# Kernel tuning notes

Measured on AMD Instinct MI355X. Metric: run time of the kernel, lower is better.

Reference implementation:

```python
import jax, jax.numpy as jnp
import numpy as np

B, S, I, H, C = 256, 128, 512, 1024, 10
VOCAB = S  # nn.Embedding(seq_length, input_dim)


def _lstm_dir(embeds_tbi, W, b):
    """Run an LSTM over time. embeds_tbi: [S,B,I]; W: [4H, I+H] stacked (g,i,f,o); b: [4H]."""
    h0 = jnp.zeros((B, H), jnp.float32)
    c0 = jnp.zeros((B, H), jnp.float32)

    def step(carry, x_t):
        c, h = carry
        xh = jnp.concatenate([x_t, h], axis=1)          # [B, I+H]
        z = xh @ W.T + b                                 # [B, 4H]
        g, i, f, o = jnp.split(z, 4, axis=1)
        g = jnp.tanh(g)
        i = jax.nn.sigmoid(i)
        f = jax.nn.sigmoid(f)
        o = jax.nn.sigmoid(o)
        new_c = g * i + c * f
        new_h = jnp.tanh(new_c) * o
        return (new_c, new_h), None

    (c_T, h_T), _ = jax.lax.scan(step, (c0, h0), embeds_tbi)
    return h_T


def setup_inputs() -> dict:
    key = jax.random.key(0)
    ks = jax.random.split(key, 8)
    x = jax.random.randint(ks[0], (B, S), 0, VOCAB)
    embed = jax.random.normal(ks[1], (VOCAB, I), jnp.float32) * 0.5
    scale = 1.0 / np.sqrt(I + H)
    fwd_W = jax.random.normal(ks[2], (4 * H, I + H), jnp.float32) * scale  # stacked g,i,f,o
    fwd_b = jax.random.normal(ks[3], (4 * H,), jnp.float32) * 0.02
    bwd_W = jax.random.normal(ks[4], (4 * H, I + H), jnp.float32) * scale
    bwd_b = jax.random.normal(ks[5], (4 * H,), jnp.float32) * 0.02
    p_w = jax.random.normal(ks[6], (C, 2 * H), jnp.float32) * (1.0 / np.sqrt(2 * H))
    p_b = jax.random.normal(ks[7], (C,), jnp.float32) * 0.02
    return {"x": x, "embed": embed, "fwd_W": fwd_W, "fwd_b": fwd_b,
            "bwd_W": bwd_W, "bwd_b": bwd_b, "p_w": p_w, "p_b": p_b}


def reference(x, embed, fwd_W, fwd_b, bwd_W, bwd_b, p_w, p_b):
    embeds = embed[x]                       # [B,S,I]
    emb_t = jnp.transpose(embeds, (1, 0, 2))  # [S,B,I]
    h_fwd = _lstm_dir(emb_t, fwd_W, fwd_b)
    h_bwd = _lstm_dir(emb_t[::-1], bwd_W, bwd_b)
    h_comb = jnp.concatenate([h_fwd, h_bwd], axis=1)  # [B,2H]
    return jax.nn.log_softmax(h_comb @ p_w.T + p_b, axis=1)
```

## Files before the change

### kernel.cpp

```cpp
#include <hip/hip_runtime.h>
#include <hip/hip_bf16.h>
#include <math.h>

#define B 256
#define S 128
#define I_DIM 512
#define H 1024
#define C 10
#define WROW 1536

#define LDS_H 131072

typedef float f32x4 __attribute__((ext_vector_type(4), may_alias));
typedef __bf16 bf16x8 __attribute__((ext_vector_type(8), may_alias));
typedef unsigned int u32x4 __attribute__((ext_vector_type(4), may_alias));
typedef unsigned long long u64;
typedef unsigned long long __attribute__((may_alias)) u64a;

__device__ __forceinline__ unsigned short f2bf(float f) {
    union { float f; unsigned u; } a; a.f = f;
    return (unsigned short)((a.u + 0x7fffu + ((a.u >> 16) & 1u)) >> 16);
}
__device__ __forceinline__ float sigf(float v) { return 1.0f / (1.0f + __expf(-v)); }
__device__ __forceinline__ float tanh_fast(float v) { return 1.0f - 2.0f / (1.0f + __expf(2.0f * v)); }

__global__ void wf_build(const float* __restrict__ fwd_W,
                         const float* __restrict__ bwd_W,
                         __hip_bfloat16* __restrict__ wF) {
    int gid = blockIdx.x * 256 + threadIdx.x;
    int lane = gid & 63, kk = (gid >> 6) & 31, nsub = (gid >> 11) & 255, d = gid >> 19;
    int n_gl = nsub * 16 + (lane & 15);
    int j = n_gl >> 2, g = n_gl & 3;
    int k = kk * 32 + (lane >> 4) * 8;
    const float* W = d ? bwd_W : fwd_W;
    const float* src = W + (size_t)(g * 1024 + j) * WROW + I_DIM + k;
    ushort4 lo = make_ushort4(f2bf(src[0]), f2bf(src[1]), f2bf(src[2]), f2bf(src[3]));
    ushort4 hi = make_ushort4(f2bf(src[4]), f2bf(src[5]), f2bf(src[6]), f2bf(src[7]));
    ushort4* dst = (ushort4*)(wF + (size_t)gid * 8);
    dst[0] = lo; dst[1] = hi;
}

__global__ void projp_kernel(const float* __restrict__ embed,
                             const float* __restrict__ fwd_W,
                             const float* __restrict__ fwd_b,
                             const float* __restrict__ bwd_W,
                             const float* __restrict__ bwd_b,
                             float* __restrict__ projP) {
    __shared__ float wrows[16][516];
    int d  = blockIdx.x >> 8;
    int nc = blockIdx.x & 255;
    int n0 = nc * 16;
    const float* W    = d ? bwd_W : fwd_W;
    const float* bias = d ? bwd_b : fwd_b;
    int tid = threadIdx.x;
    for (int idx = tid; idx < 16 * 512; idx += 256) {
        int r = idx >> 9, k = idx & 511;
        wrows[r][k] = W[(n0 + r) * WROW + k];
    }
    __syncthreads();
    for (int o = tid; o < 128 * 16; o += 256) {
        int v = o >> 4, r = o & 15;
        const float* er = embed + v * I_DIM;
        float s = bias[n0 + r];
        for (int k = 0; k < I_DIM; k++) s += er[k] * wrows[r][k];
        int n = n0 + r;
        int g = n >> 10, j = n & 1023;
        projP[(((size_t)d * 1024 + j) * 128 + v) * 4 + g] = s;
    }
}

__global__ __launch_bounds__(512, 1) void step_kernel(
        const int* __restrict__ x,
        const __hip_bfloat16* __restrict__ wF,
        const float* __restrict__ projP,
        __hip_bfloat16* __restrict__ hbuf,
        float* __restrict__ cws,
        int t) {
    extern __shared__ char smem[];
    const int bid = blockIdx.x;
    const int d = bid >> 7, bt = (bid >> 5) & 3, jt = bid & 31;
    const int tid = threadIdx.x, wid = tid >> 6, lane = tid & 63;
    const int l15 = lane & 15, l4 = lane >> 4;
    const int b0 = bt * 64;
    const size_t dBH = (size_t)d * B * H;

    if (t > 0) {
        const __hip_bfloat16* hr = hbuf + (size_t)(t & 1) * 2 * B * H + dBH + (size_t)b0 * H;
#pragma unroll
        for (int i = 0; i < 16; i++) {
            int flat = i * 512 + tid;
            int row = flat >> 7, c16 = flat & 127;
            u32x4 v = *(const u32x4*)(hr + (size_t)row * H + c16 * 8);
            *(u32x4*)(smem + row * 2048 + ((c16 * 16) ^ ((row & 7) << 4))) = v;
        }
        __syncthreads();
    }

    f32x4 acc[4] = {};
    if (t > 0) {
        const __hip_bfloat16* wp = wF + (size_t)(d * 256 + jt * 8 + wid) * 16384;
        int brow[4], bswz[4];
#pragma unroll
        for (int bs = 0; bs < 4; bs++) {
            int row = bs * 16 + l15;
            brow[bs] = row * 2048;
            bswz[bs] = (row & 7) << 4;
        }
        bf16x8 Acur = *(const bf16x8*)(wp + lane * 8);
        bf16x8 Bcur[4];
#pragma unroll
        for (int bs = 0; bs < 4; bs++)
            Bcur[bs] = *(const bf16x8*)(smem + brow[bs] + ((l4 * 16) ^ bswz[bs]));
#pragma unroll
        for (int kk = 0; kk < 32; kk++) {
            bf16x8 A = Acur;
            bf16x8 B0 = Bcur[0], B1 = Bcur[1], B2 = Bcur[2], B3 = Bcur[3];
            if (kk < 31) {
                Acur = *(const bf16x8*)(wp + (kk + 1) * 512 + lane * 8);
                int koff = (kk + 1) * 64 + l4 * 16;
#pragma unroll
                for (int bs = 0; bs < 4; bs++)
                    Bcur[bs] = *(const bf16x8*)(smem + brow[bs] + (koff ^ bswz[bs]));
            }
            acc[0] = __builtin_amdgcn_mfma_f32_16x16x32_bf16(A, B0, acc[0], 0, 0, 0);
            acc[1] = __builtin_amdgcn_mfma_f32_16x16x32_bf16(A, B1, acc[1], 0, 0, 0);
            acc[2] = __builtin_amdgcn_mfma_f32_16x16x32_bf16(A, B2, acc[2], 0, 0, 0);
            acc[3] = __builtin_amdgcn_mfma_f32_16x16x32_bf16(A, B3, acc[3], 0, 0, 0);
        }
    }

    const int tt = d ? (S - 1 - t) : t;
    const int j = jt * 32 + wid * 4 + l4;
    const f32x4* pp = (const f32x4*)projP + ((size_t)d * 1024 + j) * 128;
    f32x4 pj[4];
#pragma unroll
    for (int bs = 0; bs < 4; bs++) {
        int v = x[(b0 + bs * 16 + l15) * S + tt];
        pj[bs] = pp[v];
    }

    float* cp = cws + ((size_t)bid * 512 + tid) * 4;
    f32x4 cv = {0.f, 0.f, 0.f, 0.f};
    if (t > 0) cv = *(const f32x4*)cp;

    float hnv[4];
#pragma unroll
    for (int bs = 0; bs < 4; bs++) {
        float zg = acc[bs][0] + pj[bs][0];
        float zi = acc[bs][1] + pj[bs][1];
        float zf = acc[bs][2] + pj[bs][2];
        float zo = acc[bs][3] + pj[bs][3];
        float gg = tanh_fast(zg);
        float ii = sigf(zi);
        float ff = sigf(zf);
        float oo = sigf(zo);
        float cn = gg * ii + cv[bs] * ff;
        cv[bs] = cn;
        hnv[bs] = tanh_fast(cn) * oo;
    }
    *(f32x4*)cp = cv;

    unsigned plo = (unsigned)f2bf(hnv[0]) | ((unsigned)f2bf(hnv[1]) << 16);
    unsigned phi = (unsigned)f2bf(hnv[2]) | ((unsigned)f2bf(hnv[3]) << 16);
    unsigned short o4[4];
#pragma unroll
    for (int p = 0; p < 4; p++) {
        int src = p * 16 + l15;
        unsigned vlo = __shfl(plo, src);
        unsigned vhi = __shfl(phi, src);
        unsigned sel = (l4 < 2) ? vlo : vhi;
        o4[p] = (l4 & 1) ? (unsigned short)(sel >> 16) : (unsigned short)(sel & 0xffffu);
    }
    u64 hv = (u64)o4[0] | ((u64)o4[1] << 16) | ((u64)o4[2] << 32) | ((u64)o4[3] << 48);
    __hip_bfloat16* hw = hbuf + (size_t)((t + 1) & 1) * 2 * B * H + dBH
                         + (size_t)(b0 + lane) * H + jt * 32 + wid * 4;
    *(u64a*)hw = hv;
}

__global__ void head_kernel(const __hip_bfloat16* __restrict__ hbuf,
                            const float* __restrict__ p_w,
                            const float* __restrict__ p_b,
                            float* __restrict__ out) {
    int b = blockIdx.x;
    int lane = threadIdx.x;
    float part[C];
#pragma unroll
    for (int cc = 0; cc < C; cc++) part[cc] = 0.0f;
    for (int jj = lane; jj < 2 * H; jj += 64) {
        float hv = (jj < H)
            ? __bfloat162float(hbuf[(size_t)b * H + jj])
            : __bfloat162float(hbuf[(size_t)B * H + (size_t)b * H + jj - H]);
#pragma unroll
        for (int cc = 0; cc < C; cc++) part[cc] += hv * p_w[cc * 2 * H + jj];
    }
#pragma unroll
    for (int cc = 0; cc < C; cc++) {
        float v = part[cc];
        for (int off = 32; off; off >>= 1) v += __shfl_down(v, off);
        part[cc] = v;
    }
    if (lane == 0) {
        float lg[C];
        float m = -1e30f;
        for (int cc = 0; cc < C; cc++) {
            lg[cc] = part[cc] + p_b[cc];
            m = fmaxf(m, lg[cc]);
        }
        float s = 0.0f;
        for (int cc = 0; cc < C; cc++) s += expf(lg[cc] - m);
        float lse = logf(s) + m;
        for (int cc = 0; cc < C; cc++) out[b * C + cc] = lg[cc] - lse;
    }
}

extern "C" void kernel_launch(void* const* d_in, const int* in_sizes, int n_in,
                              void* d_out, int out_size, void* d_ws, size_t ws_size,
                              hipStream_t stream) {
    const int*   x     = (const int*)d_in[0];
    const float* embed = (const float*)d_in[1];
    const float* fwd_W = (const float*)d_in[2];
    const float* fwd_b = (const float*)d_in[3];
    const float* bwd_W = (const float*)d_in[4];
    const float* bwd_b = (const float*)d_in[5];
    const float* p_w   = (const float*)d_in[6];
    const float* p_b   = (const float*)d_in[7];
    float* outp = (float*)d_out;

    char* ws = (char*)d_ws;
    __hip_bfloat16* wF = (__hip_bfloat16*)ws;  ws += (size_t)2 * 256 * 16384 * 2;
    float* projP = (float*)ws;                 ws += (size_t)2 * 1024 * 128 * 4 * 4;
    __hip_bfloat16* hbuf = (__hip_bfloat16*)ws; ws += (size_t)2 * 2 * B * H * 2;
    float* cws = (float*)ws;                   ws += (size_t)256 * 512 * 4 * 4;

    hipLaunchKernelGGL(wf_build, dim3(4096), dim3(256), 0, stream, fwd_W, bwd_W, wF);
    hipLaunchKernelGGL(projp_kernel, dim3(512), dim3(256), 0, stream,
                       embed, fwd_W, fwd_b, bwd_W, bwd_b, projP);

    hipFuncSetAttribute((const void*)step_kernel,
                        hipFuncAttributeMaxDynamicSharedMemorySize, LDS_H);

    for (int t = 0; t < S; t++)
        hipLaunchKernelGGL(step_kernel, dim3(256), dim3(512), LDS_H, stream,
                           x, wF, projP, hbuf, cws, t);

    hipLaunchKernelGGL(head_kernel, dim3(B), dim3(64), 0, stream,
                       hbuf, p_w, p_b, outp);
}
```

Measured before the change: 1.497 ms.

## Prefetch weights deeper, hoist step loads, remap blocks across XCDs, vectorize projP

The step kernel now issues its weight loads 8 k-steps ahead through a register ring, and loads the token ids, projP rows and cell state before the h staging barrier so their global latency overlaps. Block IDs are remapped so the four batch tiles that share a weight slice land on the same XCD, which should improve L2 reuse of weights. projp_kernel is rewritten with vectorized float4 loads and register blocking over 8 vocab rows. The cost is higher register pressure in the launch_bounds(512,1) step kernel.

```diff
diff --git a/kernel.cpp b/kernel.cpp
--- a/kernel.cpp
+++ b/kernel.cpp
@@ -46,26 +46,36 @@
                              const float* __restrict__ bwd_W,
                              const float* __restrict__ bwd_b,
                              float* __restrict__ projP) {
-    __shared__ float wrows[16][516];
+    __shared__ float wrows[16][520];
     int d  = blockIdx.x >> 8;
     int nc = blockIdx.x & 255;
     int n0 = nc * 16;
     const float* W    = d ? bwd_W : fwd_W;
     const float* bias = d ? bwd_b : fwd_b;
     int tid = threadIdx.x;
-    for (int idx = tid; idx < 16 * 512; idx += 256) {
-        int r = idx >> 9, k = idx & 511;
-        wrows[r][k] = W[(n0 + r) * WROW + k];
+    for (int i = tid; i < 16 * 128; i += 256) {
+        int r = i >> 7, kc = i & 127;
+        *(f32x4*)&wrows[r][kc * 4] = *(const f32x4*)(W + (size_t)(n0 + r) * WROW + kc * 4);
     }
     __syncthreads();
-    for (int o = tid; o < 128 * 16; o += 256) {
-        int v = o >> 4, r = o & 15;
-        const float* er = embed + v * I_DIM;
-        float s = bias[n0 + r];
-        for (int k = 0; k < I_DIM; k++) s += er[k] * wrows[r][k];
-        int n = n0 + r;
-        int g = n >> 10, j = n & 1023;
-        projP[(((size_t)d * 1024 + j) * 128 + v) * 4 + g] = s;
+    const int r = tid & 15, vg = tid >> 4;
+    const float* eb = embed + (size_t)(vg * 8) * I_DIM;
+    f32x4 acc[8] = {};
+    for (int kc = 0; kc < 128; kc++) {
+        f32x4 w = *(const f32x4*)&wrows[r][kc * 4];
+#pragma unroll
+        for (int vi = 0; vi < 8; vi++) {
+            f32x4 e = *(const f32x4*)(eb + (size_t)vi * I_DIM + kc * 4);
+            acc[vi] += w * e;
+        }
+    }
+    const int n = n0 + r, g = n >> 10, j = n & 1023;
+    const float bv = bias[n];
+    float* outp = projP + ((size_t)d * 1024 + j) * 128 * 4 + g;
+#pragma unroll
+    for (int vi = 0; vi < 8; vi++) {
+        float s = acc[vi][0] + acc[vi][1] + acc[vi][2] + acc[vi][3] + bv;
+        outp[(vg * 8 + vi) * 4] = s;
     }
 }
 
@@ -78,11 +88,32 @@
         int t) {
     extern __shared__ char smem[];
     const int bid = blockIdx.x;
-    const int d = bid >> 7, bt = (bid >> 5) & 3, jt = bid & 31;
+    const int xcd = bid & 7, idx = bid >> 3;
+    const int slot = idx >> 2, bt = idx & 3;
+    const int grp = slot * 8 + xcd;
+    const int d = grp >> 5, jt = grp & 31;
     const int tid = threadIdx.x, wid = tid >> 6, lane = tid & 63;
     const int l15 = lane & 15, l4 = lane >> 4;
     const int b0 = bt * 64;
     const size_t dBH = (size_t)d * B * H;
+
+    const __hip_bfloat16* wp = wF + (size_t)(d * 256 + jt * 8 + wid) * 16384;
+
+    bf16x8 Ap[8];
+    if (t > 0) {
+#pragma unroll
+        for (int p = 0; p < 8; p++)
+            Ap[p] = *(const bf16x8*)(wp + p * 512 + lane * 8);
+    }
+    const int tt = d ? (S - 1 - t) : t;
+    int vv[4];
+#pragma unroll
+    for (int bs = 0; bs < 4; bs++)
+        vv[bs] = x[(b0 + bs * 16 + l15) * S + tt];
+
+    float* cp = cws + ((size_t)bid * 512 + tid) * 4;
+    f32x4 cv = {0.f, 0.f, 0.f, 0.f};
+    if (t > 0) cv = *(const f32x4*)cp;
 
     if (t > 0) {
         const __hip_bfloat16* hr = hbuf + (size_t)(t & 1) * 2 * B * H + dBH + (size_t)b0 * H;
@@ -93,12 +124,17 @@
             u32x4 v = *(const u32x4*)(hr + (size_t)row * H + c16 * 8);
             *(u32x4*)(smem + row * 2048 + ((c16 * 16) ^ ((row & 7) << 4))) = v;
         }
-        __syncthreads();
-    }
+    }
+
+    const int j = jt * 32 + wid * 4 + l4;
+    const f32x4* pp = (const f32x4*)projP + ((size_t)d * 1024 + j) * 128;
+    f32x4 pj[4];
+#pragma unroll
+    for (int bs = 0; bs < 4; bs++) pj[bs] = pp[vv[bs]];
 
     f32x4 acc[4] = {};
     if (t > 0) {
-        const __hip_bfloat16* wp = wF + (size_t)(d * 256 + jt * 8 + wid) * 16384;
+        __syncthreads();
         int brow[4], bswz[4];
 #pragma unroll
         for (int bs = 0; bs < 4; bs++) {
@@ -106,17 +142,17 @@
             brow[bs] = row * 2048;
             bswz[bs] = (row & 7) << 4;
         }
-        bf16x8 Acur = *(const bf16x8*)(wp + lane * 8);
         bf16x8 Bcur[4];
 #pragma unroll
         for (int bs = 0; bs < 4; bs++)
             Bcur[bs] = *(const bf16x8*)(smem + brow[bs] + ((l4 * 16) ^ bswz[bs]));
 #pragma unroll
         for (int kk = 0; kk < 32; kk++) {
-            bf16x8 A = Acur;
+            bf16x8 A = Ap[kk & 7];
+            if (kk < 24)
+                Ap[kk & 7] = *(const bf16x8*)(wp + (kk + 8) * 512 + lane * 8);
             bf16x8 B0 = Bcur[0], B1 = Bcur[1], B2 = Bcur[2], B3 = Bcur[3];
             if (kk < 31) {
-                Acur = *(const bf16x8*)(wp + (kk + 1) * 512 + lane * 8);
                 int koff = (kk + 1) * 64 + l4 * 16;
 #pragma unroll
                 for (int bs = 0; bs < 4; bs++)
@@ -128,20 +164,6 @@
             acc[3] = __builtin_amdgcn_mfma_f32_16x16x32_bf16(A, B3, acc[3], 0, 0, 0);
         }
     }
-
-    const int tt = d ? (S - 1 - t) : t;
-    const int j = jt * 32 + wid * 4 + l4;
-    const f32x4* pp = (const f32x4*)projP + ((size_t)d * 1024 + j) * 128;
-    f32x4 pj[4];
-#pragma unroll
-    for (int bs = 0; bs < 4; bs++) {
-        int v = x[(b0 + bs * 16 + l15) * S + tt];
-        pj[bs] = pp[v];
-    }
-
-    float* cp = cws + ((size_t)bid * 512 + tid) * 4;
-    f32x4 cv = {0.f, 0.f, 0.f, 0.f};
-    if (t > 0) cv = *(const f32x4*)cp;
 
     float hnv[4];
 #pragma unroll
```

Result: slower. 1.554 ms (+3.8%).

## Replace per-step launches with persistent cooperative BiLSTM kernel and MFMA input projection

Applied to the files above, without the earlier changes.

The 128 per-timestep kernel launches become one cooperative persistent kernel. Each workgroup handles both directions over a 32-row batch tile, keeps cell state in registers, and syncs with other workgroups through per-batch-tile global flag counters and LDS counters, so no grid-wide barrier is used. The input projection is rebuilt as an MFMA kernel that splits the embeddings into bf16 hi/lo parts to keep near-fp32 accuracy. This is meant to remove launch overhead and the global round trips for cell state. The cost is spin-wait synchronisation, a dependence on all workgroups being co-resident, and less work per wave.

```diff
diff --git a/kernel.cpp b/kernel.cpp
--- a/kernel.cpp
+++ b/kernel.cpp
@@ -9,17 +9,20 @@
 #define C 10
 #define WROW 1536
 
-#define LDS_H 131072
+#define LDS_MAIN 131200
 
 typedef float f32x4 __attribute__((ext_vector_type(4), may_alias));
 typedef __bf16 bf16x8 __attribute__((ext_vector_type(8), may_alias));
 typedef unsigned int u32x4 __attribute__((ext_vector_type(4), may_alias));
 typedef unsigned long long u64;
-typedef unsigned long long __attribute__((may_alias)) u64a;
 
 __device__ __forceinline__ unsigned short f2bf(float f) {
     union { float f; unsigned u; } a; a.f = f;
     return (unsigned short)((a.u + 0x7fffu + ((a.u >> 16) & 1u)) >> 16);
+}
+__device__ __forceinline__ float bf2f(unsigned short b) {
+    union { unsigned u; float f; } a; a.u = ((unsigned)b) << 16;
+    return a.f;
 }
 __device__ __forceinline__ float sigf(float v) { return 1.0f / (1.0f + __expf(-v)); }
 __device__ __forceinline__ float tanh_fast(float v) { return 1.0f - 2.0f / (1.0f + __expf(2.0f * v)); }
@@ -40,141 +43,288 @@
     dst[0] = lo; dst[1] = hi;
 }
 
-__global__ void projp_kernel(const float* __restrict__ embed,
-                             const float* __restrict__ fwd_W,
-                             const float* __restrict__ fwd_b,
-                             const float* __restrict__ bwd_W,
-                             const float* __restrict__ bwd_b,
-                             float* __restrict__ projP) {
-    __shared__ float wrows[16][516];
-    int d  = blockIdx.x >> 8;
-    int nc = blockIdx.x & 255;
-    int n0 = nc * 16;
-    const float* W    = d ? bwd_W : fwd_W;
-    const float* bias = d ? bwd_b : fwd_b;
-    int tid = threadIdx.x;
-    for (int idx = tid; idx < 16 * 512; idx += 256) {
-        int r = idx >> 9, k = idx & 511;
-        wrows[r][k] = W[(n0 + r) * WROW + k];
+__global__ void wxf_build(const float* __restrict__ fwd_W,
+                          const float* __restrict__ bwd_W,
+                          __hip_bfloat16* __restrict__ wxF) {
+    int gid = blockIdx.x * 256 + threadIdx.x;
+    int lane = gid & 63, kk = (gid >> 6) & 15, nsub = (gid >> 10) & 255, d = gid >> 18;
+    int n_gl = nsub * 16 + (lane & 15);
+    int j = n_gl >> 2, g = n_gl & 3;
+    int k = kk * 32 + (lane >> 4) * 8;
+    const float* W = d ? bwd_W : fwd_W;
+    const float* src = W + (size_t)(g * 1024 + j) * WROW + k;
+    ushort4 lo = make_ushort4(f2bf(src[0]), f2bf(src[1]), f2bf(src[2]), f2bf(src[3]));
+    ushort4 hi = make_ushort4(f2bf(src[4]), f2bf(src[5]), f2bf(src[6]), f2bf(src[7]));
+    ushort4* dst = (ushort4*)(wxF + (size_t)gid * 8);
+    dst[0] = lo; dst[1] = hi;
+}
+
+__global__ void ehl_build(const float* __restrict__ embed,
+                          unsigned short* __restrict__ ehl) {
+    int idx = blockIdx.x * 256 + threadIdx.x;
+    float e = embed[idx];
+    unsigned short hb = f2bf(e);
+    unsigned short lb = f2bf(e - bf2f(hb));
+    ehl[idx] = hb;
+    ehl[65536 + idx] = lb;
+}
+
+__global__ __launch_bounds__(256) void projp_mfma(
+        const __hip_bfloat16* __restrict__ wxF,
+        const unsigned short* __restrict__ ehl,
+        const float* __restrict__ fwd_b,
+        const float* __restrict__ bwd_b,
+        float* __restrict__ projP) {
+    extern __shared__ char sm[];
+    const int bid = blockIdx.x;
+    const int d = bid >> 7, jt = (bid >> 2) & 31, vb = bid & 3;
+    const int tid = threadIdx.x, w = tid >> 6, lane = tid & 63;
+    const int l15 = lane & 15, l4 = lane >> 4;
+    const int v0 = vb * 32;
+
+    for (int i = 0; i < 16; i++) {
+        int chunk = i * 256 + tid;
+        int row = chunk >> 6, c16 = chunk & 63;
+        int p = row >> 5, vs = v0 + (row & 31);
+        u32x4 vd = *(const u32x4*)(ehl + ((size_t)p * 128 + vs) * 512 + c16 * 8);
+        *(u32x4*)(sm + row * 1024 + ((c16 * 16) ^ ((row & 7) << 4))) = vd;
     }
     __syncthreads();
-    for (int o = tid; o < 128 * 16; o += 256) {
-        int v = o >> 4, r = o & 15;
-        const float* er = embed + v * I_DIM;
-        float s = bias[n0 + r];
-        for (int k = 0; k < I_DIM; k++) s += er[k] * wrows[r][k];
-        int n = n0 + r;
-        int g = n >> 10, j = n & 1023;
-        projP[(((size_t)d * 1024 + j) * 128 + v) * 4 + g] = s;
-    }
-}
-
-__global__ __launch_bounds__(512, 1) void step_kernel(
+
+    const __hip_bfloat16* ap0 = wxF + ((size_t)((d * 256 + jt * 8 + w * 2 + 0) * 16)) * 512;
+    const __hip_bfloat16* ap1 = wxF + ((size_t)((d * 256 + jt * 8 + w * 2 + 1) * 16)) * 512;
+    int hrow[2], hswz[2], lrow[2], lswz[2];
+#pragma unroll
+    for (int vt = 0; vt < 2; vt++) {
+        int hr = vt * 16 + l15, lr = hr + 32;
+        hrow[vt] = hr * 1024; hswz[vt] = (hr & 7) << 4;
+        lrow[vt] = lr * 1024; lswz[vt] = (lr & 7) << 4;
+    }
+    f32x4 acc[2][2] = {};
+#pragma unroll
+    for (int kk = 0; kk < 16; kk++) {
+        bf16x8 A0 = *(const bf16x8*)(ap0 + kk * 512 + lane * 8);
+        bf16x8 A1 = *(const bf16x8*)(ap1 + kk * 512 + lane * 8);
+        int ko = kk * 64 + l4 * 16;
+        bf16x8 Bh0 = *(const bf16x8*)(sm + hrow[0] + (ko ^ hswz[0]));
+        bf16x8 Bh1 = *(const bf16x8*)(sm + hrow[1] + (ko ^ hswz[1]));
+        bf16x8 Bl0 = *(const bf16x8*)(sm + lrow[0] + (ko ^ lswz[0]));
+        bf16x8 Bl1 = *(const bf16x8*)(sm + lrow[1] + (ko ^ lswz[1]));
+        acc[0][0] = __builtin_amdgcn_mfma_f32_16x16x32_bf16(A0, Bh0, acc[0][0], 0, 0, 0);
+        acc[0][0] = __builtin_amdgcn_mfma_f32_16x16x32_bf16(A0, Bl0, acc[0][0], 0, 0, 0);
+        acc[0][1] = __builtin_amdgcn_mfma_f32_16x16x32_bf16(A0, Bh1, acc[0][1], 0, 0, 0);
+        acc[0][1] = __builtin_amdgcn_mfma_f32_16x16x32_bf16(A0, Bl1, acc[0][1], 0, 0, 0);
+        acc[1][0] = __builtin_amdgcn_mfma_f32_16x16x32_bf16(A1, Bh0, acc[1][0], 0, 0, 0);
+        acc[1][0] = __builtin_amdgcn_mfma_f32_16x16x32_bf16(A1, Bl0, acc[1][0], 0, 0, 0);
+        acc[1][1] = __builtin_amdgcn_mfma_f32_16x16x32_bf16(A1, Bh1, acc[1][1], 0, 0, 0);
+        acc[1][1] = __builtin_amdgcn_mfma_f32_16x16x32_bf16(A1, Bl1, acc[1][1], 0, 0, 0);
+    }
+    const float* bp = d ? bwd_b : fwd_b;
+#pragma unroll
+    for (int nt = 0; nt < 2; nt++) {
+        int j = jt * 32 + w * 8 + nt * 4 + l4;
+        f32x4 bv = { bp[j], bp[1024 + j], bp[2048 + j], bp[3072 + j] };
+#pragma unroll
+        for (int vt = 0; vt < 2; vt++) {
+            int v = v0 + vt * 16 + l15;
+            *(f32x4*)(projP + ((size_t)(d * 1024 + j) * 128 + v) * 4) = acc[nt][vt] + bv;
+        }
+    }
+}
+
+__device__ __forceinline__ void stage_batch(const __hip_bfloat16* hr, char* dst,
+                                            int r0, int cc, int ibase) {
+    const void* p0 = (const void*)(hr + (size_t)(ibase + 0 + r0) * H + cc * 8);
+    const void* p1 = (const void*)(hr + (size_t)(ibase + 2 + r0) * H + cc * 8);
+    const void* p2 = (const void*)(hr + (size_t)(ibase + 4 + r0) * H + cc * 8);
+    const void* p3 = (const void*)(hr + (size_t)(ibase + 6 + r0) * H + cc * 8);
+    const void* p4 = (const void*)(hr + (size_t)(ibase + 8 + r0) * H + cc * 8);
+    const void* p5 = (const void*)(hr + (size_t)(ibase + 10 + r0) * H + cc * 8);
+    const void* p6 = (const void*)(hr + (size_t)(ibase + 12 + r0) * H + cc * 8);
+    const void* p7 = (const void*)(hr + (size_t)(ibase + 14 + r0) * H + cc * 8);
+    u32x4 s0, s1, s2, s3, s4, s5, s6, s7;
+    asm volatile(
+        "global_load_dwordx4 %0, %8, off sc0 sc1\n\t"
+        "global_load_dwordx4 %1, %9, off sc0 sc1\n\t"
+        "global_load_dwordx4 %2, %10, off sc0 sc1\n\t"
+        "global_load_dwordx4 %3, %11, off sc0 sc1\n\t"
+        "global_load_dwordx4 %4, %12, off sc0 sc1\n\t"
+        "global_load_dwordx4 %5, %13, off sc0 sc1\n\t"
+        "global_load_dwordx4 %6, %14, off sc0 sc1\n\t"
+        "global_load_dwordx4 %7, %15, off sc0 sc1\n\t"
+        "s_waitcnt vmcnt(0)"
+        : "=&v"(s0), "=&v"(s1), "=&v"(s2), "=&v"(s3),
+          "=&v"(s4), "=&v"(s5), "=&v"(s6), "=&v"(s7)
+        : "v"(p0), "v"(p1), "v"(p2), "v"(p3), "v"(p4), "v"(p5), "v"(p6), "v"(p7)
+        : "memory");
+    int row;
+    row = ibase + 0 + r0;  *(u32x4*)(dst + row * 2048 + ((cc * 16) ^ ((row & 7) << 4))) = s0;
+    row = ibase + 2 + r0;  *(u32x4*)(dst + row * 2048 + ((cc * 16) ^ ((row & 7) << 4))) = s1;
+    row = ibase + 4 + r0;  *(u32x4*)(dst + row * 2048 + ((cc * 16) ^ ((row & 7) << 4))) = s2;
+    row = ibase + 6 + r0;  *(u32x4*)(dst + row * 2048 + ((cc * 16) ^ ((row & 7) << 4))) = s3;
+    row = ibase + 8 + r0;  *(u32x4*)(dst + row * 2048 + ((cc * 16) ^ ((row & 7) << 4))) = s4;
+    row = ibase + 10 + r0; *(u32x4*)(dst + row * 2048 + ((cc * 16) ^ ((row & 7) << 4))) = s5;
+    row = ibase + 12 + r0; *(u32x4*)(dst + row * 2048 + ((cc * 16) ^ ((row & 7) << 4))) = s6;
+    row = ibase + 14 + r0; *(u32x4*)(dst + row * 2048 + ((cc * 16) ^ ((row & 7) << 4))) = s7;
+}
+
+__global__ __launch_bounds__(512, 2) void bilstm_persistent(
         const int* __restrict__ x,
         const __hip_bfloat16* __restrict__ wF,
         const float* __restrict__ projP,
         __hip_bfloat16* __restrict__ hbuf,
-        float* __restrict__ cws,
-        int t) {
+        unsigned* __restrict__ flags) {
     extern __shared__ char smem[];
+    unsigned* cnt = (unsigned*)(smem + 131072);
     const int bid = blockIdx.x;
-    const int d = bid >> 7, bt = (bid >> 5) & 3, jt = bid & 31;
-    const int tid = threadIdx.x, wid = tid >> 6, lane = tid & 63;
+    const int bt = bid >> 5, jt = bid & 31;
+    const int tid = threadIdx.x;
+    const int d = tid >> 8;
+    const int tid2 = tid & 255;
+    const int w = tid2 >> 6, lane = tid & 63;
     const int l15 = lane & 15, l4 = lane >> 4;
-    const int b0 = bt * 64;
+    const int b0 = bt * 32;
     const size_t dBH = (size_t)d * B * H;
-
-    if (t > 0) {
-        const __hip_bfloat16* hr = hbuf + (size_t)(t & 1) * 2 * B * H + dBH + (size_t)b0 * H;
-#pragma unroll
-        for (int i = 0; i < 16; i++) {
-            int flat = i * 512 + tid;
-            int row = flat >> 7, c16 = flat & 127;
-            u32x4 v = *(const u32x4*)(hr + (size_t)row * H + c16 * 8);
-            *(u32x4*)(smem + row * 2048 + ((c16 * 16) ^ ((row & 7) << 4))) = v;
-        }
-        __syncthreads();
-    }
-
-    f32x4 acc[4] = {};
-    if (t > 0) {
-        const __hip_bfloat16* wp = wF + (size_t)(d * 256 + jt * 8 + wid) * 16384;
-        int brow[4], bswz[4];
-#pragma unroll
-        for (int bs = 0; bs < 4; bs++) {
-            int row = bs * 16 + l15;
-            brow[bs] = row * 2048;
-            bswz[bs] = (row & 7) << 4;
-        }
-        bf16x8 Acur = *(const bf16x8*)(wp + lane * 8);
-        bf16x8 Bcur[4];
-#pragma unroll
-        for (int bs = 0; bs < 4; bs++)
-            Bcur[bs] = *(const bf16x8*)(smem + brow[bs] + ((l4 * 16) ^ bswz[bs]));
-#pragma unroll
-        for (int kk = 0; kk < 32; kk++) {
-            bf16x8 A = Acur;
-            bf16x8 B0 = Bcur[0], B1 = Bcur[1], B2 = Bcur[2], B3 = Bcur[3];
-            if (kk < 31) {
-                Acur = *(const bf16x8*)(wp + (kk + 1) * 512 + lane * 8);
-                int koff = (kk + 1) * 64 + l4 * 16;
-#pragma unroll
-                for (int bs = 0; bs < 4; bs++)
-                    Bcur[bs] = *(const bf16x8*)(smem + brow[bs] + (koff ^ bswz[bs]));
+    char* btile = smem + d * 65536;
+
+    if (tid < 4) cnt[tid] = 0;
+    __syncthreads();
+
+    const __hip_bfloat16* wp = wF + ((size_t)((d * 256 + jt * 8 + w * 2) * 32)) * 512;
+    int brow[2], bswz[2];
+#pragma unroll
+    for (int bs = 0; bs < 2; bs++) {
+        int row = bs * 16 + l15;
+        brow[bs] = row * 2048;
+        bswz[bs] = (row & 7) << 4;
+    }
+    const int jbase = jt * 32 + w * 8;
+    const int r0 = tid2 >> 7, cc = tid2 & 127;
+    unsigned* flagp = flags + (size_t)(d * 8 + bt) * 16;
+
+    float cst[2][2] = {};
+    int vv[2];
+    f32x4 pj[2][2];
+    {
+        int tt = d ? (S - 1) : 0;
+        vv[0] = x[(b0 + l15) * S + tt];
+        vv[1] = x[(b0 + 16 + l15) * S + tt];
+#pragma unroll
+        for (int nt = 0; nt < 2; nt++) {
+            int j = jbase + nt * 4 + l4;
+            const float* pb = projP + (size_t)(d * 1024 + j) * 128 * 4;
+            pj[nt][0] = *(const f32x4*)(pb + vv[0] * 4);
+            pj[nt][1] = *(const f32x4*)(pb + vv[1] * 4);
+        }
+    }
+
+    for (int t = 0; t < S; t++) {
+        bf16x8 Ap[2][4];
+        if (t > 0) {
+#pragma unroll
+            for (int p = 0; p < 4; p++) {
+                Ap[0][p] = *(const bf16x8*)(wp + (0 * 32 + p) * 512 + lane * 8);
+                Ap[1][p] = *(const bf16x8*)(wp + (1 * 32 + p) * 512 + lane * 8);
             }
-            acc[0] = __builtin_amdgcn_mfma_f32_16x16x32_bf16(A, B0, acc[0], 0, 0, 0);
-            acc[1] = __builtin_amdgcn_mfma_f32_16x16x32_bf16(A, B1, acc[1], 0, 0, 0);
-            acc[2] = __builtin_amdgcn_mfma_f32_16x16x32_bf16(A, B2, acc[2], 0, 0, 0);
-            acc[3] = __builtin_amdgcn_mfma_f32_16x16x32_bf16(A, B3, acc[3], 0, 0, 0);
-        }
-    }
-
-    const int tt = d ? (S - 1 - t) : t;
-    const int j = jt * 32 + wid * 4 + l4;
-    const f32x4* pp = (const f32x4*)projP + ((size_t)d * 1024 + j) * 128;
-    f32x4 pj[4];
-#pragma unroll
-    for (int bs = 0; bs < 4; bs++) {
-        int v = x[(b0 + bs * 16 + l15) * S + tt];
-        pj[bs] = pp[v];
-    }
-
-    float* cp = cws + ((size_t)bid * 512 + tid) * 4;
-    f32x4 cv = {0.f, 0.f, 0.f, 0.f};
-    if (t > 0) cv = *(const f32x4*)cp;
-
-    float hnv[4];
-#pragma unroll
-    for (int bs = 0; bs < 4; bs++) {
-        float zg = acc[bs][0] + pj[bs][0];
-        float zi = acc[bs][1] + pj[bs][1];
-        float zf = acc[bs][2] + pj[bs][2];
-        float zo = acc[bs][3] + pj[bs][3];
-        float gg = tanh_fast(zg);
-        float ii = sigf(zi);
-        float ff = sigf(zf);
-        float oo = sigf(zo);
-        float cn = gg * ii + cv[bs] * ff;
-        cv[bs] = cn;
-        hnv[bs] = tanh_fast(cn) * oo;
-    }
-    *(f32x4*)cp = cv;
-
-    unsigned plo = (unsigned)f2bf(hnv[0]) | ((unsigned)f2bf(hnv[1]) << 16);
-    unsigned phi = (unsigned)f2bf(hnv[2]) | ((unsigned)f2bf(hnv[3]) << 16);
-    unsigned short o4[4];
-#pragma unroll
-    for (int p = 0; p < 4; p++) {
-        int src = p * 16 + l15;
-        unsigned vlo = __shfl(plo, src);
-        unsigned vhi = __shfl(phi, src);
-        unsigned sel = (l4 < 2) ? vlo : vhi;
-        o4[p] = (l4 & 1) ? (unsigned short)(sel >> 16) : (unsigned short)(sel & 0xffffu);
-    }
-    u64 hv = (u64)o4[0] | ((u64)o4[1] << 16) | ((u64)o4[2] << 32) | ((u64)o4[3] << 48);
-    __hip_bfloat16* hw = hbuf + (size_t)((t + 1) & 1) * 2 * B * H + dBH
-                         + (size_t)(b0 + lane) * H + jt * 32 + wid * 4;
-    *(u64a*)hw = hv;
+            if (lane == 0) {
+                while (__hip_atomic_load(flagp, __ATOMIC_RELAXED,
+                                         __HIP_MEMORY_SCOPE_AGENT) < 32u * (unsigned)t)
+                    __builtin_amdgcn_s_sleep(2);
+            }
+            asm volatile("" ::: "memory");
+            const __hip_bfloat16* hr = hbuf + (size_t)(t & 1) * 2 * B * H + dBH + (size_t)b0 * H;
+            stage_batch(hr, btile, r0, cc, 0);
+            stage_batch(hr, btile, r0, cc, 16);
+            if (lane == 0)
+                __hip_atomic_fetch_add(&cnt[2 + d], 1u, __ATOMIC_RELAXED,
+                                       __HIP_MEMORY_SCOPE_WORKGROUP);
+            while (__hip_atomic_load(&cnt[2 + d], __ATOMIC_RELAXED,
+                                     __HIP_MEMORY_SCOPE_WORKGROUP) < 4u * (unsigned)t)
+                __builtin_amdgcn_s_sleep(1);
+            asm volatile("" ::: "memory");
+        }
+
+        f32x4 acc[2][2] = {};
+        if (t > 0) {
+            bf16x8 Bc0 = *(const bf16x8*)(btile + brow[0] + ((l4 * 16) ^ bswz[0]));
+            bf16x8 Bc1 = *(const bf16x8*)(btile + brow[1] + ((l4 * 16) ^ bswz[1]));
+#pragma unroll
+            for (int kk = 0; kk < 32; kk++) {
+                bf16x8 A0 = Ap[0][kk & 3], A1 = Ap[1][kk & 3];
+                bf16x8 B0 = Bc0, B1 = Bc1;
+                if (kk < 28) {
+                    Ap[0][kk & 3] = *(const bf16x8*)(wp + (0 * 32 + kk + 4) * 512 + lane * 8);
+                    Ap[1][kk & 3] = *(const bf16x8*)(wp + (1 * 32 + kk + 4) * 512 + lane * 8);
+                }
+                if (kk < 31) {
+                    int koff = (kk + 1) * 64 + l4 * 16;
+                    Bc0 = *(const bf16x8*)(btile + brow[0] + (koff ^ bswz[0]));
+                    Bc1 = *(const bf16x8*)(btile + brow[1] + (koff ^ bswz[1]));
+                }
+                acc[0][0] = __builtin_amdgcn_mfma_f32_16x16x32_bf16(A0, B0, acc[0][0], 0, 0, 0);
+                acc[0][1] = __builtin_amdgcn_mfma_f32_16x16x32_bf16(A0, B1, acc[0][1], 0, 0, 0);
+                acc[1][0] = __builtin_amdgcn_mfma_f32_16x16x32_bf16(A1, B0, acc[1][0], 0, 0, 0);
+                acc[1][1] = __builtin_amdgcn_mfma_f32_16x16x32_bf16(A1, B1, acc[1][1], 0, 0, 0);
+            }
+        }
+
+        float hn[2][2];
+#pragma unroll
+        for (int nt = 0; nt < 2; nt++)
+#pragma unroll
+            for (int bs = 0; bs < 2; bs++) {
+                float zg = acc[nt][bs][0] + pj[nt][bs][0];
+                float zi = acc[nt][bs][1] + pj[nt][bs][1];
+                float zf = acc[nt][bs][2] + pj[nt][bs][2];
+                float zo = acc[nt][bs][3] + pj[nt][bs][3];
+                float gg = tanh_fast(zg);
+                float ii = sigf(zi);
+                float ff = sigf(zf);
+                float oo = sigf(zo);
+                float cn = gg * ii + cst[nt][bs] * ff;
+                cst[nt][bs] = cn;
+                hn[nt][bs] = tanh_fast(cn) * oo;
+            }
+
+        unsigned pk0 = (unsigned)f2bf(hn[0][0]) | ((unsigned)f2bf(hn[0][1]) << 16);
+        unsigned pk1 = (unsigned)f2bf(hn[1][0]) | ((unsigned)f2bf(hn[1][1]) << 16);
+        unsigned sv[8];
+#pragma unroll
+        for (int q = 0; q < 8; q++) {
+            unsigned pk = (q < 4) ? pk0 : pk1;
+            unsigned s = __shfl(pk, (q & 3) * 16 + l15);
+            sv[q] = (lane & 16) ? (s >> 16) : (s & 0xffffu);
+        }
+        if (lane < 32) {
+            u32x4 hv = { sv[0] | (sv[1] << 16), sv[2] | (sv[3] << 16),
+                         sv[4] | (sv[5] << 16), sv[6] | (sv[7] << 16) };
+            void* hw = (void*)(hbuf + (size_t)((t + 1) & 1) * 2 * B * H + dBH
+                               + (size_t)(b0 + lane) * H + jbase);
+            asm volatile("global_store_dwordx4 %0, %1, off sc0 sc1"
+                         :: "v"(hw), "v"(hv) : "memory");
+        }
+        asm volatile("s_waitcnt vmcnt(0)" ::: "memory");
+        if (lane == 0) {
+            unsigned old = __hip_atomic_fetch_add(&cnt[d], 1u, __ATOMIC_RELAXED,
+                                                  __HIP_MEMORY_SCOPE_WORKGROUP);
+            if (old == 4u * (unsigned)t + 3u)
+                __hip_atomic_fetch_add(flagp, 1u, __ATOMIC_RELAXED,
+                                       __HIP_MEMORY_SCOPE_AGENT);
+        }
+
+        if (t + 1 < S) {
+            int tt = d ? (S - 2 - t) : (t + 1);
+            vv[0] = x[(b0 + l15) * S + tt];
+            vv[1] = x[(b0 + 16 + l15) * S + tt];
+#pragma unroll
+            for (int nt = 0; nt < 2; nt++) {
+                int j = jbase + nt * 4 + l4;
+                const float* pb = projP + (size_t)(d * 1024 + j) * 128 * 4;
+                pj[nt][0] = *(const f32x4*)(pb + vv[0] * 4);
+                pj[nt][1] = *(const f32x4*)(pb + vv[1] * 4);
+            }
+        }
+    }
 }
 
 __global__ void head_kernel(const __hip_bfloat16* __restrict__ hbuf,
@@ -185,31 +335,31 @@
     int lane = threadIdx.x;
     float part[C];
 #pragma unroll
-    for (int cc = 0; cc < C; cc++) part[cc] = 0.0f;
+    for (int cc2 = 0; cc2 < C; cc2++) part[cc2] = 0.0f;
     for (int jj = lane; jj < 2 * H; jj += 64) {
         float hv = (jj < H)
             ? __bfloat162float(hbuf[(size_t)b * H + jj])
             : __bfloat162float(hbuf[(size_t)B * H + (size_t)b * H + jj - H]);
 #pragma unroll
-        for (int cc = 0; cc < C; cc++) part[cc] += hv * p_w[cc * 2 * H + jj];
-    }
-#pragma unroll
-    for (int cc = 0; cc < C; cc++) {
-        float v = part[cc];
+        for (int cc2 = 0; cc2 < C; cc2++) part[cc2] += hv * p_w[cc2 * 2 * H + jj];
+    }
+#pragma unroll
+    for (int cc2 = 0; cc2 < C; cc2++) {
+        float v = part[cc2];
         for (int off = 32; off; off >>= 1) v += __shfl_down(v, off);
-        part[cc] = v;
+        part[cc2] = v;
     }
     if (lane == 0) {
         float lg[C];
         float m = -1e30f;
-        for (int cc = 0; cc < C; cc++) {
-            lg[cc] = part[cc] + p_b[cc];
-            m = fmaxf(m, lg[cc]);
+        for (int cc2 = 0; cc2 < C; cc2++) {
+            lg[cc2] = part[cc2] + p_b[cc2];
+            m = fmaxf(m, lg[cc2]);
         }
         float s = 0.0f;
-        for (int cc = 0; cc < C; cc++) s += expf(lg[cc] - m);
+        for (int cc2 = 0; cc2 < C; cc2++) s += expf(lg[cc2] - m);
         float lse = logf(s) + m;
-        for (int cc = 0; cc < C; cc++) out[b * C + cc] = lg[cc] - lse;
+        for (int cc2 = 0; cc2 < C; cc2++) out[b * C + cc2] = lg[cc2] - lse;
     }
 }
 
@@ -227,21 +377,28 @@
     float* outp = (float*)d_out;
 
     char* ws = (char*)d_ws;
-    __hip_bfloat16* wF = (__hip_bfloat16*)ws;  ws += (size_t)2 * 256 * 16384 * 2;
-    float* projP = (float*)ws;                 ws += (size_t)2 * 1024 * 128 * 4 * 4;
+    __hip_bfloat16* wF  = (__hip_bfloat16*)ws;  ws += (size_t)2 * 256 * 16384 * 2;
+    __hip_bfloat16* wxF = (__hip_bfloat16*)ws;  ws += (size_t)2 * 256 * 8192 * 2;
+    unsigned short* ehl = (unsigned short*)ws;  ws += (size_t)2 * 128 * 512 * 2;
+    float* projP = (float*)ws;                  ws += (size_t)2 * 1024 * 128 * 4 * 4;
     __hip_bfloat16* hbuf = (__hip_bfloat16*)ws; ws += (size_t)2 * 2 * B * H * 2;
-    float* cws = (float*)ws;                   ws += (size_t)256 * 512 * 4 * 4;
-
+    unsigned* flags = (unsigned*)ws;            ws += (size_t)2 * 8 * 16 * 4;
+
+    hipMemsetAsync(flags, 0, (size_t)2 * 8 * 16 * 4, stream);
     hipLaunchKernelGGL(wf_build, dim3(4096), dim3(256), 0, stream, fwd_W, bwd_W, wF);
-    hipLaunchKernelGGL(projp_kernel, dim3(512), dim3(256), 0, stream,
-                       embed, fwd_W, fwd_b, bwd_W, bwd_b, projP);
-
-    hipFuncSetAttribute((const void*)step_kernel,
-                        hipFuncAttributeMaxDynamicSharedMemorySize, LDS_H);
-
-    for (int t = 0; t < S; t++)
-        hipLaunchKernelGGL(step_kernel, dim3(256), dim3(512), LDS_H, stream,
-                           x, wF, projP, hbuf, cws, t);
+    hipLaunchKernelGGL(wxf_build, dim3(2048), dim3(256), 0, stream, fwd_W, bwd_W, wxF);
+    hipLaunchKernelGGL(ehl_build, dim3(256), dim3(256), 0, stream, embed, ehl);
+
+    hipFuncSetAttribute((const void*)projp_mfma,
+                        hipFuncAttributeMaxDynamicSharedMemorySize, 65536);
+    hipLaunchKernelGGL(projp_mfma, dim3(256), dim3(256), 65536, stream,
+                       wxF, ehl, fwd_b, bwd_b, projP);
+
+    hipFuncSetAttribute((const void*)bilstm_persistent,
+                        hipFuncAttributeMaxDynamicSharedMemorySize, LDS_MAIN);
+    void* args[] = {(void*)&x, (void*)&wF, (void*)&projP, (void*)&hbuf, (void*)&flags};
+    hipLaunchCooperativeKernel((void*)bilstm_persistent, dim3(256), dim3(512),
+                               args, LDS_MAIN, stream);
 
     hipLaunchKernelGGL(head_kernel, dim3(B), dim3(64), 0, stream,
                        hbuf, p_w, p_b, outp);
```

New measurement: 2.749 ms. 1.84x slower.
